# Kernel optimization log

Hardware: AMD Instinct MI355X
Metric: run time of the kernel (lower is better)

Reference implementation:

```python
import jax, jax.numpy as jnp
import numpy as np

TAU = 0.4
EPS = 1e-8


def setup_inputs() -> dict:
    key = jax.random.key(0)
    k1, k2 = jax.random.split(key)
    B, N, C, M = 4, 4096, 256, 2048
    l_feat = jax.random.normal(k1, (B, N, C), dtype=jnp.float32)
    g_feat = jax.random.normal(k2, (B, C, M), dtype=jnp.float32)
    return {"l_feat": l_feat, "g_feat": g_feat}


def reference(l_feat, g_feat):
    # l_feat: [B, N, C], g_feat: [B, C, M]
    # cosine similarity over channel dim C (torch CosineSimilarity, dim=2)
    l_norm = jnp.linalg.norm(l_feat, axis=2)          # [B, N]
    g_norm = jnp.linalg.norm(g_feat, axis=1)          # [B, M]
    dot = jnp.einsum('bnc,bcm->bnm', l_feat, g_feat)  # [B, N, M]
    cos_sim = dot / jnp.maximum(l_norm[:, :, None] * g_norm[:, None, :], EPS)
    sim = jnp.exp(cos_sim / TAU)                      # [B, N, M]
    # diag_embed(rowsum) followed by linalg.inv and bmm is exactly
    # row-wise division by the degree (row sum)
    sim = sim / jnp.sum(sim, axis=2, keepdims=True)
    # bmm(sim, g_feat^T): [B,N,M] x [B,M,C] -> [B,N,C]
    g_enh = jnp.einsum('bnm,bcm->bnc', sim, g_feat)
    return l_feat + g_enh
```

## Files before the change

kernel.cpp:

```cpp
#include <hip/hip_runtime.h>

#define B_ 4
#define N_ 4096
#define C_ 256
#define M_ 2048

typedef __attribute__((ext_vector_type(8))) short short8;
typedef __attribute__((ext_vector_type(4))) short short4v;
typedef __attribute__((ext_vector_type(4))) float f32x4;

union U16x8 { uint4 u4; unsigned short us[8]; short8 s8; };
union U16x4 { uint2 u2; unsigned short us[4]; short4v s4; };

__device__ __forceinline__ float bf2f(unsigned short h) {
    unsigned int u = ((unsigned int)h) << 16;
    return __builtin_bit_cast(float, u);
}
__device__ __forceinline__ unsigned short f2bf(float f) {
    unsigned int u = __builtin_bit_cast(unsigned int, f);
    u += 0x7FFFu + ((u >> 16) & 1u);
    return (unsigned short)(u >> 16);
}

#define GLB_AS(p) ((const __attribute__((address_space(1))) unsigned int*)(p))
#define LDS_AS(p) ((__attribute__((address_space(3))) unsigned int*)(p))

__device__ __forceinline__ f32x4 mfma16x16(short4v a, short4v b, f32x4 c) {
#if __has_builtin(__builtin_amdgcn_mfma_f32_16x16x16bf16_1k)
    return __builtin_amdgcn_mfma_f32_16x16x16bf16_1k(a, b, c, 0, 0, 0);
#else
    asm("v_mfma_f32_16x16x16_bf16 %0, %1, %2, %0" : "+v"(c) : "v"(a), "v"(b));
    return c;
#endif
}

__global__ __launch_bounds__(1024) void k_prep(const float* __restrict__ g,
                                               unsigned short* __restrict__ gcm,
                                               unsigned short* __restrict__ gmc) {
    __shared__ float red[16][64];
    __shared__ float sInv[64];
    __shared__ unsigned short T[64 * 66];
    const int b = blockIdx.y, m0 = blockIdx.x * 64;
    const int tid = threadIdx.x;
    const int ml = tid & 63, cq = tid >> 6;

    const float* gb = g + (size_t)b * C_ * M_ + m0 + ml;
    float ss = 0.f;
#pragma unroll 4
    for (int i = 0; i < 16; ++i) {
        float v = gb[(size_t)(cq * 16 + i) * M_];
        ss += v * v;
    }
    red[cq][ml] = ss;
    __syncthreads();
    if (cq == 0) {
        float t = 0.f;
#pragma unroll
        for (int k = 0; k < 16; ++k) t += red[k][ml];
        sInv[ml] = 1.f / fmaxf(sqrtf(t), 1e-8f);
    }
    __syncthreads();

    for (int c0 = 0; c0 < C_; c0 += 64) {
        const float* gbase = g + ((size_t)b * C_ + c0) * M_ + m0;
        unsigned short* gcmb = gcm + ((size_t)b * C_ + c0) * M_ + m0;
        {
            int id = tid;
            int ci = id >> 4, mq = (id & 15) * 4;
            float4 v = *(const float4*)(gbase + (size_t)ci * M_ + mq);
            uint2 pk;
            pk.x = (unsigned)f2bf(v.x) | ((unsigned)f2bf(v.y) << 16);
            pk.y = (unsigned)f2bf(v.z) | ((unsigned)f2bf(v.w) << 16);
            *(uint2*)(gcmb + (size_t)ci * M_ + mq) = pk;
            T[ci * 66 + mq + 0] = f2bf(v.x * sInv[mq + 0]);
            T[ci * 66 + mq + 1] = f2bf(v.y * sInv[mq + 1]);
            T[ci * 66 + mq + 2] = f2bf(v.z * sInv[mq + 2]);
            T[ci * 66 + mq + 3] = f2bf(v.w * sInv[mq + 3]);
        }
        __syncthreads();
        unsigned short* gmcb = gmc + ((size_t)b * M_ + m0) * C_ + c0;
        if (tid < 512) {
            int mr = tid >> 3, cc8 = (tid & 7) * 8;
            U16x8 t;
#pragma unroll
            for (int k = 0; k < 8; ++k) t.us[k] = T[(cc8 + k) * 66 + mr];
            *(uint4*)(gmcb + (size_t)mr * C_ + cc8) = t.u4;
        }
        __syncthreads();
    }
}

__global__ __launch_bounds__(512, 2) void k_main(
    const float* __restrict__ l,
    const unsigned short* __restrict__ gcm,
    const unsigned short* __restrict__ gmc,
    float* __restrict__ out)
{
    __shared__ __align__(16) char sMem[66560];
    unsigned short* sGmc = (unsigned short*)sMem;
    unsigned short* sGcm = (unsigned short*)(sMem + 32768);
    float (*sDen)[64] = (float (*)[64])(sMem + 65536);

    const int tid = threadIdx.x;
    const int w = tid >> 6;
    const int lane = tid & 63;
    const int l15 = lane & 15;
    const int quad = lane >> 4;
    const int kh = w & 3;
    const int rh = w >> 2;

    const int bid = blockIdx.x;
    const int xcd = bid & 7;
    const int b = xcd >> 1;
    const int row0 = (((bid >> 3) << 1) | (xcd & 1)) * 64;

    int goffA[4], goffB[4];
#pragma unroll
    for (int i = 0; i < 4; ++i) {
        int p = (w * 4 + i) * 64 + lane;
        int rA = p >> 5;
        goffA[i] = rA * 256 + (((p & 31) ^ (rA & 31)) << 3);
        int rB = p >> 3;
        goffB[i] = rB * 2048 + (((p & 7) ^ ((rB >> 1) & 7)) << 3);
    }

    const unsigned short* gmc_b = gmc + (size_t)b * M_ * C_;
    const unsigned short* gcm_b = gcm + (size_t)b * C_ * M_;

    auto dmaA = [&](int m0) {
#pragma unroll
        for (int i = 0; i < 4; ++i)
            __builtin_amdgcn_global_load_lds(GLB_AS(gmc_b + (size_t)m0 * 256 + goffA[i]),
                                             LDS_AS(&sGmc[(w * 4 + i) * 512]), 16, 0, 0);
    };
    auto dmaB = [&](int m0) {
#pragma unroll
        for (int i = 0; i < 4; ++i)
            __builtin_amdgcn_global_load_lds(GLB_AS(gcm_b + (size_t)m0 + goffB[i]),
                                             LDS_AS(&sGcm[(w * 4 + i) * 512]), 16, 0, 0);
    };

    dmaA(0);
    dmaB(0);

    short8 qf[2][8];
#pragma unroll
    for (int rt = 0; rt < 2; ++rt) {
        const float* lrow = l + ((size_t)b * N_ + row0 + rh * 32 + rt * 16 + l15) * C_;
        U16x8 qt[8];
        float ss = 0.f;
#pragma unroll
        for (int kk = 0; kk < 8; ++kk) {
            float4 x0 = *(const float4*)(lrow + kk * 32 + quad * 8);
            float4 x1 = *(const float4*)(lrow + kk * 32 + quad * 8 + 4);
            ss += x0.x*x0.x + x0.y*x0.y + x0.z*x0.z + x0.w*x0.w;
            ss += x1.x*x1.x + x1.y*x1.y + x1.z*x1.z + x1.w*x1.w;
            qt[kk].us[0] = f2bf(x0.x); qt[kk].us[1] = f2bf(x0.y);
            qt[kk].us[2] = f2bf(x0.z); qt[kk].us[3] = f2bf(x0.w);
            qt[kk].us[4] = f2bf(x1.x); qt[kk].us[5] = f2bf(x1.y);
            qt[kk].us[6] = f2bf(x1.z); qt[kk].us[7] = f2bf(x1.w);
        }
        ss += __shfl_xor(ss, 16);
        ss += __shfl_xor(ss, 32);
        const float invl = 1.0f / fmaxf(sqrtf(ss), 1e-8f);
#pragma unroll
        for (int kk = 0; kk < 8; ++kk) {
            U16x8 t;
#pragma unroll
            for (int j = 0; j < 8; ++j) t.us[j] = f2bf(bf2f(qt[kk].us[j]) * invl);
            qf[rt][kk] = t.s8;
        }
    }

    __syncthreads();

    f32x4 zero = {0.f, 0.f, 0.f, 0.f};
    f32x4 o[2][16];
#pragma unroll
    for (int i = 0; i < 2; ++i)
#pragma unroll
        for (int j = 0; j < 16; ++j) o[i][j] = zero;
    float dl0 = 0.f, dl1 = 0.f;

    const unsigned short* gAbase = &sGmc[(kh * 16 + l15) * 256];
    const int rxor = (kh * 16 + l15) & 31;
    const int chunkXor = (kh * 4 + quad) ^ (l15 & 14);
    const unsigned short* gBbase = &sGcm[l15 * 64 + (chunkXor << 2)];

    for (int mt = 0; mt < 32; ++mt) {
        f32x4 sa0 = zero, sa1 = zero;
#pragma unroll
        for (int kk = 0; kk < 8; ++kk) {
            short8 ag = *(const short8*)&gAbase[((kk * 4 + quad) ^ rxor) << 3];
            sa0 = __builtin_amdgcn_mfma_f32_16x16x32_bf16(ag, qf[0][kk], sa0, 0, 0, 0);
            sa1 = __builtin_amdgcn_mfma_f32_16x16x32_bf16(ag, qf[1][kk], sa1, 0, 0, 0);
        }
        U16x4 pk0, pk1;
#pragma unroll
        for (int r = 0; r < 4; ++r) {
            float p0 = exp2f(sa0[r] * 3.6067376022224085f);
            float p1 = exp2f(sa1[r] * 3.6067376022224085f);
            dl0 += p0; dl1 += p1;
            pk0.us[r] = f2bf(p0);
            pk1.us[r] = f2bf(p1);
        }
        __syncthreads();
        if (mt < 31) dmaA((mt + 1) * 64);

#pragma unroll
        for (int ct = 0; ct < 16; ++ct) {
            short4v bb = *(const short4v*)&gBbase[ct * 1024];
            o[0][ct] = mfma16x16(pk0.s4, bb, o[0][ct]);
            o[1][ct] = mfma16x16(pk1.s4, bb, o[1][ct]);
        }
        __syncthreads();
        if (mt < 31) dmaB((mt + 1) * 64);
    }

    {
        float d0 = dl0;
        d0 += __shfl_xor(d0, 16);
        d0 += __shfl_xor(d0, 32);
        float d1 = dl1;
        d1 += __shfl_xor(d1, 16);
        d1 += __shfl_xor(d1, 32);
        if (quad == 0) {
            sDen[kh][rh * 32 + l15] = d0;
            sDen[kh][rh * 32 + 16 + l15] = d1;
        }
    }

    f32x4* red4 = (f32x4*)sMem;
    const int wslot = kh * 1024 + quad * 16 + l15;
    const int rslot = (4 * kh) * 64 + quad * 16 + l15;
    f32x4 oacc0[4], oacc1[4];

#define RED_ROUND(RH, OSRC, ODST)                                              \
    __syncthreads();                                                           \
    if (rh == (RH)) {                                                          \
        _Pragma("unroll")                                                      \
        for (int j = 0; j < 16; ++j) red4[wslot + j * 64] = OSRC[j];           \
    }                                                                          \
    __syncthreads();                                                           \
    if (rh == (RH)) {                                                          \
        _Pragma("unroll")                                                      \
        for (int jj = 0; jj < 4; ++jj) {                                       \
            const int base = rslot + jj * 64;                                  \
            ODST[jj] = red4[base] + red4[base + 1024] +                        \
                       red4[base + 2048] + red4[base + 3072];                  \
        }                                                                      \
    }

    RED_ROUND(0, o[0], oacc0)
    RED_ROUND(0, o[1], oacc1)
    RED_ROUND(1, o[0], oacc0)
    RED_ROUND(1, o[1], oacc1)
#undef RED_ROUND

    const float* lb = l + ((size_t)b * N_ + row0 + rh * 32) * C_;
    float* ob = out + ((size_t)b * N_ + row0 + rh * 32) * C_;
#pragma unroll
    for (int r = 0; r < 4; ++r) {
        {
            const int row = quad * 4 + r;
            const int grow = rh * 32 + row;
            const float inv = 1.f / (sDen[0][grow] + sDen[1][grow] + sDen[2][grow] + sDen[3][grow]);
            const size_t rb = (size_t)row * C_;
#pragma unroll
            for (int jj = 0; jj < 4; ++jj) {
                const int c = kh * 64 + jj * 16 + l15;
                ob[rb + c] = lb[rb + c] + oacc0[jj][r] * inv;
            }
        }
        {
            const int row = 16 + quad * 4 + r;
            const int grow = rh * 32 + row;
            const float inv = 1.f / (sDen[0][grow] + sDen[1][grow] + sDen[2][grow] + sDen[3][grow]);
            const size_t rb = (size_t)row * C_;
#pragma unroll
            for (int jj = 0; jj < 4; ++jj) {
                const int c = kh * 64 + jj * 16 + l15;
                ob[rb + c] = lb[rb + c] + oacc1[jj][r] * inv;
            }
        }
    }
}

extern "C" void kernel_launch(void* const* d_in, const int* in_sizes, int n_in,
                              void* d_out, int out_size, void* d_ws, size_t ws_size,
                              hipStream_t stream) {
    (void)in_sizes; (void)n_in; (void)out_size; (void)ws_size;
    const float* l = (const float*)d_in[0];
    const float* g = (const float*)d_in[1];
    float* outp = (float*)d_out;

    char* ws = (char*)d_ws;
    unsigned short* gmc = (unsigned short*)ws;
    unsigned short* gcm = (unsigned short*)(ws + (size_t)B_ * M_ * C_ * 2);

    k_prep<<<dim3(M_ / 64, B_), 1024, 0, stream>>>(g, gcm, gmc);
    k_main<<<dim3(N_ / 64 * B_), 512, 0, stream>>>(l, gcm, gmc, outp);
}
```

Measured before the change: 136.9 us.

## Double-buffer LDS tiles and drop one barrier per iteration

Doubles the shared-memory staging so the next two m-tiles of g (both layouts) are prefetched into alternate buffers while the current tile is consumed. This removes the mid-iteration barrier and gives the async global-to-LDS loads a full iteration of lead time. The LDS footprint roughly doubles, so launch bounds drop to one block per CU. That gives up occupancy but allows more registers per thread, which matters little since the grid is only about one block per CU.

```diff
diff --git a/kernel.cpp b/kernel.cpp
--- a/kernel.cpp
+++ b/kernel.cpp
@@ -90,16 +90,16 @@
     }
 }
 
-__global__ __launch_bounds__(512, 2) void k_main(
+__global__ __launch_bounds__(512, 1) void k_main(
     const float* __restrict__ l,
     const unsigned short* __restrict__ gcm,
     const unsigned short* __restrict__ gmc,
     float* __restrict__ out)
 {
-    __shared__ __align__(16) char sMem[66560];
-    unsigned short* sGmc = (unsigned short*)sMem;
-    unsigned short* sGcm = (unsigned short*)(sMem + 32768);
-    float (*sDen)[64] = (float (*)[64])(sMem + 65536);
+    __shared__ __align__(16) char sMem[132096];
+    unsigned short* sGmcD = (unsigned short*)sMem;
+    unsigned short* sGcmD = (unsigned short*)(sMem + 65536);
+    float (*sDen)[64] = (float (*)[64])(sMem + 131072);
 
     const int tid = threadIdx.x;
     const int w = tid >> 6;
@@ -127,21 +127,23 @@
     const unsigned short* gmc_b = gmc + (size_t)b * M_ * C_;
     const unsigned short* gcm_b = gcm + (size_t)b * C_ * M_;
 
-    auto dmaA = [&](int m0) {
+    auto dmaA = [&](int tile, int buf) {
 #pragma unroll
         for (int i = 0; i < 4; ++i)
-            __builtin_amdgcn_global_load_lds(GLB_AS(gmc_b + (size_t)m0 * 256 + goffA[i]),
-                                             LDS_AS(&sGmc[(w * 4 + i) * 512]), 16, 0, 0);
+            __builtin_amdgcn_global_load_lds(GLB_AS(gmc_b + (size_t)tile * 16384 + goffA[i]),
+                                             LDS_AS(&sGmcD[buf * 16384 + (w * 4 + i) * 512]), 16, 0, 0);
     };
-    auto dmaB = [&](int m0) {
+    auto dmaB = [&](int tile, int buf) {
 #pragma unroll
         for (int i = 0; i < 4; ++i)
-            __builtin_amdgcn_global_load_lds(GLB_AS(gcm_b + (size_t)m0 + goffB[i]),
-                                             LDS_AS(&sGcm[(w * 4 + i) * 512]), 16, 0, 0);
+            __builtin_amdgcn_global_load_lds(GLB_AS(gcm_b + (size_t)tile * 64 + goffB[i]),
+                                             LDS_AS(&sGcmD[buf * 16384 + (w * 4 + i) * 512]), 16, 0, 0);
     };
 
-    dmaA(0);
-    dmaB(0);
+    dmaA(0, 0);
+    dmaB(0, 0);
+    dmaA(1, 1);
+    dmaB(1, 1);
 
     short8 qf[2][8];
 #pragma unroll
@@ -182,16 +184,20 @@
         for (int j = 0; j < 16; ++j) o[i][j] = zero;
     float dl0 = 0.f, dl1 = 0.f;
 
-    const unsigned short* gAbase = &sGmc[(kh * 16 + l15) * 256];
+    const unsigned short* gAbase = &sGmcD[(kh * 16 + l15) * 256];
     const int rxor = (kh * 16 + l15) & 31;
     const int chunkXor = (kh * 4 + quad) ^ (l15 & 14);
-    const unsigned short* gBbase = &sGcm[l15 * 64 + (chunkXor << 2)];
+    const unsigned short* gBbase = &sGcmD[l15 * 64 + (chunkXor << 2)];
 
     for (int mt = 0; mt < 32; ++mt) {
+        const int cur = mt & 1;
+        const unsigned short* gA = gAbase + cur * 16384;
+        const unsigned short* gB = gBbase + cur * 16384;
+
         f32x4 sa0 = zero, sa1 = zero;
 #pragma unroll
         for (int kk = 0; kk < 8; ++kk) {
-            short8 ag = *(const short8*)&gAbase[((kk * 4 + quad) ^ rxor) << 3];
+            short8 ag = *(const short8*)&gA[((kk * 4 + quad) ^ rxor) << 3];
             sa0 = __builtin_amdgcn_mfma_f32_16x16x32_bf16(ag, qf[0][kk], sa0, 0, 0, 0);
             sa1 = __builtin_amdgcn_mfma_f32_16x16x32_bf16(ag, qf[1][kk], sa1, 0, 0, 0);
         }
@@ -204,17 +210,19 @@
             pk0.us[r] = f2bf(p0);
             pk1.us[r] = f2bf(p1);
         }
-        __syncthreads();
-        if (mt < 31) dmaA((mt + 1) * 64);
 
 #pragma unroll
         for (int ct = 0; ct < 16; ++ct) {
-            short4v bb = *(const short4v*)&gBbase[ct * 1024];
+            short4v bb = *(const short4v*)&gB[ct * 1024];
             o[0][ct] = mfma16x16(pk0.s4, bb, o[0][ct]);
             o[1][ct] = mfma16x16(pk1.s4, bb, o[1][ct]);
         }
+
         __syncthreads();
-        if (mt < 31) dmaB((mt + 1) * 64);
+        if (mt < 30) {
+            dmaA(mt + 2, cur);
+            dmaB(mt + 2, cur);
+        }
     }
 
     {
```

New measurement: 144.0 us. +5.2%, slower.

## Use 1024-thread blocks with 16 rows per wave to halve register tiles

Applied to the files above, without the earlier changes.

Doubles k_main's block size to 16 waves so that each wave handles 16 query rows instead of 32. This halves per-wave accumulators, Q fragments and DMA work, and splits the cross-wave reduction into four rounds. The aim is lower register pressure and more waves to hide latency, at the cost of less reuse of each LDS B/A fragment per MFMA and more reduction barriers. The launch bounds of (1024,4) may force register spills, and LDS usage of 66.5KB per block caps residency.

```diff
diff --git a/kernel.cpp b/kernel.cpp
--- a/kernel.cpp
+++ b/kernel.cpp
@@ -90,7 +90,7 @@
     }
 }
 
-__global__ __launch_bounds__(512, 2) void k_main(
+__global__ __launch_bounds__(1024, 4) void k_main(
     const float* __restrict__ l,
     const unsigned short* __restrict__ gcm,
     const unsigned short* __restrict__ gmc,
@@ -114,10 +114,10 @@
     const int b = xcd >> 1;
     const int row0 = (((bid >> 3) << 1) | (xcd & 1)) * 64;
 
-    int goffA[4], goffB[4];
-#pragma unroll
-    for (int i = 0; i < 4; ++i) {
-        int p = (w * 4 + i) * 64 + lane;
+    int goffA[2], goffB[2];
+#pragma unroll
+    for (int i = 0; i < 2; ++i) {
+        int p = (w * 2 + i) * 64 + lane;
         int rA = p >> 5;
         goffA[i] = rA * 256 + (((p & 31) ^ (rA & 31)) << 3);
         int rB = p >> 3;
@@ -129,24 +129,23 @@
 
     auto dmaA = [&](int m0) {
 #pragma unroll
-        for (int i = 0; i < 4; ++i)
+        for (int i = 0; i < 2; ++i)
             __builtin_amdgcn_global_load_lds(GLB_AS(gmc_b + (size_t)m0 * 256 + goffA[i]),
-                                             LDS_AS(&sGmc[(w * 4 + i) * 512]), 16, 0, 0);
+                                             LDS_AS(&sGmc[(w * 2 + i) * 512]), 16, 0, 0);
     };
     auto dmaB = [&](int m0) {
 #pragma unroll
-        for (int i = 0; i < 4; ++i)
+        for (int i = 0; i < 2; ++i)
             __builtin_amdgcn_global_load_lds(GLB_AS(gcm_b + (size_t)m0 + goffB[i]),
-                                             LDS_AS(&sGcm[(w * 4 + i) * 512]), 16, 0, 0);
+                                             LDS_AS(&sGcm[(w * 2 + i) * 512]), 16, 0, 0);
     };
 
     dmaA(0);
     dmaB(0);
 
-    short8 qf[2][8];
-#pragma unroll
-    for (int rt = 0; rt < 2; ++rt) {
-        const float* lrow = l + ((size_t)b * N_ + row0 + rh * 32 + rt * 16 + l15) * C_;
+    short8 qf[8];
+    {
+        const float* lrow = l + ((size_t)b * N_ + row0 + rh * 16 + l15) * C_;
         U16x8 qt[8];
         float ss = 0.f;
 #pragma unroll
@@ -168,19 +167,17 @@
             U16x8 t;
 #pragma unroll
             for (int j = 0; j < 8; ++j) t.us[j] = f2bf(bf2f(qt[kk].us[j]) * invl);
-            qf[rt][kk] = t.s8;
+            qf[kk] = t.s8;
         }
     }
 
     __syncthreads();
 
     f32x4 zero = {0.f, 0.f, 0.f, 0.f};
-    f32x4 o[2][16];
-#pragma unroll
-    for (int i = 0; i < 2; ++i)
-#pragma unroll
-        for (int j = 0; j < 16; ++j) o[i][j] = zero;
-    float dl0 = 0.f, dl1 = 0.f;
+    f32x4 o[16];
+#pragma unroll
+    for (int j = 0; j < 16; ++j) o[j] = zero;
+    float dl = 0.f;
 
     const unsigned short* gAbase = &sGmc[(kh * 16 + l15) * 256];
     const int rxor = (kh * 16 + l15) & 31;
@@ -188,21 +185,18 @@
     const unsigned short* gBbase = &sGcm[l15 * 64 + (chunkXor << 2)];
 
     for (int mt = 0; mt < 32; ++mt) {
-        f32x4 sa0 = zero, sa1 = zero;
+        f32x4 sa = zero;
 #pragma unroll
         for (int kk = 0; kk < 8; ++kk) {
             short8 ag = *(const short8*)&gAbase[((kk * 4 + quad) ^ rxor) << 3];
-            sa0 = __builtin_amdgcn_mfma_f32_16x16x32_bf16(ag, qf[0][kk], sa0, 0, 0, 0);
-            sa1 = __builtin_amdgcn_mfma_f32_16x16x32_bf16(ag, qf[1][kk], sa1, 0, 0, 0);
-        }
-        U16x4 pk0, pk1;
+            sa = __builtin_amdgcn_mfma_f32_16x16x32_bf16(ag, qf[kk], sa, 0, 0, 0);
+        }
+        U16x4 pk;
 #pragma unroll
         for (int r = 0; r < 4; ++r) {
-            float p0 = exp2f(sa0[r] * 3.6067376022224085f);
-            float p1 = exp2f(sa1[r] * 3.6067376022224085f);
-            dl0 += p0; dl1 += p1;
-            pk0.us[r] = f2bf(p0);
-            pk1.us[r] = f2bf(p1);
+            float p = exp2f(sa[r] * 3.6067376022224085f);
+            dl += p;
+            pk.us[r] = f2bf(p);
         }
         __syncthreads();
         if (mt < 31) dmaA((mt + 1) * 64);
@@ -210,78 +204,58 @@
 #pragma unroll
         for (int ct = 0; ct < 16; ++ct) {
             short4v bb = *(const short4v*)&gBbase[ct * 1024];
-            o[0][ct] = mfma16x16(pk0.s4, bb, o[0][ct]);
-            o[1][ct] = mfma16x16(pk1.s4, bb, o[1][ct]);
+            o[ct] = mfma16x16(pk.s4, bb, o[ct]);
         }
         __syncthreads();
         if (mt < 31) dmaB((mt + 1) * 64);
     }
 
     {
-        float d0 = dl0;
-        d0 += __shfl_xor(d0, 16);
-        d0 += __shfl_xor(d0, 32);
-        float d1 = dl1;
-        d1 += __shfl_xor(d1, 16);
-        d1 += __shfl_xor(d1, 32);
-        if (quad == 0) {
-            sDen[kh][rh * 32 + l15] = d0;
-            sDen[kh][rh * 32 + 16 + l15] = d1;
-        }
+        float d = dl;
+        d += __shfl_xor(d, 16);
+        d += __shfl_xor(d, 32);
+        if (quad == 0) sDen[kh][rh * 16 + l15] = d;
     }
 
     f32x4* red4 = (f32x4*)sMem;
     const int wslot = kh * 1024 + quad * 16 + l15;
     const int rslot = (4 * kh) * 64 + quad * 16 + l15;
-    f32x4 oacc0[4], oacc1[4];
-
-#define RED_ROUND(RH, OSRC, ODST)                                              \
+    f32x4 oacc[4];
+
+#define RED_ROUND(RH)                                                          \
     __syncthreads();                                                           \
     if (rh == (RH)) {                                                          \
         _Pragma("unroll")                                                      \
-        for (int j = 0; j < 16; ++j) red4[wslot + j * 64] = OSRC[j];           \
+        for (int j = 0; j < 16; ++j) red4[wslot + j * 64] = o[j];              \
     }                                                                          \
     __syncthreads();                                                           \
     if (rh == (RH)) {                                                          \
         _Pragma("unroll")                                                      \
         for (int jj = 0; jj < 4; ++jj) {                                       \
             const int base = rslot + jj * 64;                                  \
-            ODST[jj] = red4[base] + red4[base + 1024] +                        \
+            oacc[jj] = red4[base] + red4[base + 1024] +                        \
                        red4[base + 2048] + red4[base + 3072];                  \
         }                                                                      \
     }
 
-    RED_ROUND(0, o[0], oacc0)
-    RED_ROUND(0, o[1], oacc1)
-    RED_ROUND(1, o[0], oacc0)
-    RED_ROUND(1, o[1], oacc1)
+    RED_ROUND(0)
+    RED_ROUND(1)
+    RED_ROUND(2)
+    RED_ROUND(3)
 #undef RED_ROUND
 
-    const float* lb = l + ((size_t)b * N_ + row0 + rh * 32) * C_;
-    float* ob = out + ((size_t)b * N_ + row0 + rh * 32) * C_;
+    const float* lb = l + ((size_t)b * N_ + row0 + rh * 16) * C_;
+    float* ob = out + ((size_t)b * N_ + row0 + rh * 16) * C_;
 #pragma unroll
     for (int r = 0; r < 4; ++r) {
-        {
-            const int row = quad * 4 + r;
-            const int grow = rh * 32 + row;
-            const float inv = 1.f / (sDen[0][grow] + sDen[1][grow] + sDen[2][grow] + sDen[3][grow]);
-            const size_t rb = (size_t)row * C_;
-#pragma unroll
-            for (int jj = 0; jj < 4; ++jj) {
-                const int c = kh * 64 + jj * 16 + l15;
-                ob[rb + c] = lb[rb + c] + oacc0[jj][r] * inv;
-            }
-        }
-        {
-            const int row = 16 + quad * 4 + r;
-            const int grow = rh * 32 + row;
-            const float inv = 1.f / (sDen[0][grow] + sDen[1][grow] + sDen[2][grow] + sDen[3][grow]);
-            const size_t rb = (size_t)row * C_;
-#pragma unroll
-            for (int jj = 0; jj < 4; ++jj) {
-                const int c = kh * 64 + jj * 16 + l15;
-                ob[rb + c] = lb[rb + c] + oacc1[jj][r] * inv;
-            }
+        const int row = quad * 4 + r;
+        const int grow = rh * 16 + row;
+        const float inv = 1.f / (sDen[0][grow] + sDen[1][grow] + sDen[2][grow] + sDen[3][grow]);
+        const size_t rb = (size_t)row * C_;
+#pragma unroll
+        for (int jj = 0; jj < 4; ++jj) {
+            const int c = kh * 64 + jj * 16 + l15;
+            ob[rb + c] = lb[rb + c] + oacc[jj][r] * inv;
         }
     }
 }
@@ -299,5 +273,5 @@
     unsigned short* gcm = (unsigned short*)(ws + (size_t)B_ * M_ * C_ * 2);
 
     k_prep<<<dim3(M_ / 64, B_), 1024, 0, stream>>>(g, gcm, gmc);
-    k_main<<<dim3(N_ / 64 * B_), 512, 0, stream>>>(l, gcm, gmc, outp);
-}
+    k_main<<<dim3(N_ / 64 * B_), 1024, 0, stream>>>(l, gcm, gmc, outp);
+}
```

Result: slower. 147.3 us (+7.7%).

## Pre-swizzle g into MFMA fragment layout and read operands directly from global

Applied to the files above, without the earlier changes.

The prep kernel now writes both bf16 copies of g in a layout blocked to match the MFMA fragment order. The main kernel drops the LDS staging (global_load_lds DMA plus two barriers per tile) and loads A and B fragments straight from global memory, relying on L2/L1 caching. This removes per-iteration synchronisation but exposes global load latency in the inner loop without explicit prefetch. Launch bounds are relaxed to one block per CU.

```diff
diff --git a/kernel.cpp b/kernel.cpp
--- a/kernel.cpp
+++ b/kernel.cpp
@@ -21,9 +21,6 @@
     u += 0x7FFFu + ((u >> 16) & 1u);
     return (unsigned short)(u >> 16);
 }
-
-#define GLB_AS(p) ((const __attribute__((address_space(1))) unsigned int*)(p))
-#define LDS_AS(p) ((__attribute__((address_space(3))) unsigned int*)(p))
 
 __device__ __forceinline__ f32x4 mfma16x16(short4v a, short4v b, f32x4 c) {
 #if __has_builtin(__builtin_amdgcn_mfma_f32_16x16x16bf16_1k)
@@ -35,8 +32,8 @@
 }
 
 __global__ __launch_bounds__(1024) void k_prep(const float* __restrict__ g,
-                                               unsigned short* __restrict__ gcm,
-                                               unsigned short* __restrict__ gmc) {
+                                               unsigned short* __restrict__ gcm2,
+                                               unsigned short* __restrict__ gmc2) {
     __shared__ float red[16][64];
     __shared__ float sInv[64];
     __shared__ unsigned short T[64 * 66];
@@ -61,44 +58,45 @@
     }
     __syncthreads();
 
+    unsigned short* gmc2b = gmc2 + (size_t)b * 524288 + (size_t)blockIdx.x * 16384;
+    unsigned short* gcm2b = gcm2 + (size_t)b * 524288 + (size_t)blockIdx.x * 16384;
+
     for (int c0 = 0; c0 < C_; c0 += 64) {
         const float* gbase = g + ((size_t)b * C_ + c0) * M_ + m0;
-        unsigned short* gcmb = gcm + ((size_t)b * C_ + c0) * M_ + m0;
         {
-            int id = tid;
-            int ci = id >> 4, mq = (id & 15) * 4;
+            int ci = tid >> 4, mq = (tid & 15) * 4;
             float4 v = *(const float4*)(gbase + (size_t)ci * M_ + mq);
             uint2 pk;
             pk.x = (unsigned)f2bf(v.x) | ((unsigned)f2bf(v.y) << 16);
             pk.y = (unsigned)f2bf(v.z) | ((unsigned)f2bf(v.w) << 16);
-            *(uint2*)(gcmb + (size_t)ci * M_ + mq) = pk;
+            const int cg = c0 + ci;
+            *(uint2*)(gcm2b + (cg >> 4) * 1024 + (mq >> 4) * 256 + (cg & 15) * 16 +
+                      ((mq >> 2) & 3) * 4) = pk;
             T[ci * 66 + mq + 0] = f2bf(v.x * sInv[mq + 0]);
             T[ci * 66 + mq + 1] = f2bf(v.y * sInv[mq + 1]);
             T[ci * 66 + mq + 2] = f2bf(v.z * sInv[mq + 2]);
             T[ci * 66 + mq + 3] = f2bf(v.w * sInv[mq + 3]);
         }
         __syncthreads();
-        unsigned short* gmcb = gmc + ((size_t)b * M_ + m0) * C_ + c0;
         if (tid < 512) {
             int mr = tid >> 3, cc8 = (tid & 7) * 8;
-            U16x8 t;
-#pragma unroll
-            for (int k = 0; k < 8; ++k) t.us[k] = T[(cc8 + k) * 66 + mr];
-            *(uint4*)(gmcb + (size_t)mr * C_ + cc8) = t.u4;
+            U16x8 t8;
+#pragma unroll
+            for (int k = 0; k < 8; ++k) t8.us[k] = T[(cc8 + k) * 66 + mr];
+            const int cg = c0 + cc8;
+            *(uint4*)(gmc2b + (cg >> 5) * 2048 + mr * 32 + ((cg >> 3) & 3) * 8) = t8.u4;
         }
         __syncthreads();
     }
 }
 
-__global__ __launch_bounds__(512, 2) void k_main(
+__global__ __launch_bounds__(512, 1) void k_main(
     const float* __restrict__ l,
-    const unsigned short* __restrict__ gcm,
-    const unsigned short* __restrict__ gmc,
+    const unsigned short* __restrict__ gcm2,
+    const unsigned short* __restrict__ gmc2,
     float* __restrict__ out)
 {
     __shared__ __align__(16) char sMem[66560];
-    unsigned short* sGmc = (unsigned short*)sMem;
-    unsigned short* sGcm = (unsigned short*)(sMem + 32768);
     float (*sDen)[64] = (float (*)[64])(sMem + 65536);
 
     const int tid = threadIdx.x;
@@ -114,34 +112,8 @@
     const int b = xcd >> 1;
     const int row0 = (((bid >> 3) << 1) | (xcd & 1)) * 64;
 
-    int goffA[4], goffB[4];
-#pragma unroll
-    for (int i = 0; i < 4; ++i) {
-        int p = (w * 4 + i) * 64 + lane;
-        int rA = p >> 5;
-        goffA[i] = rA * 256 + (((p & 31) ^ (rA & 31)) << 3);
-        int rB = p >> 3;
-        goffB[i] = rB * 2048 + (((p & 7) ^ ((rB >> 1) & 7)) << 3);
-    }
-
-    const unsigned short* gmc_b = gmc + (size_t)b * M_ * C_;
-    const unsigned short* gcm_b = gcm + (size_t)b * C_ * M_;
-
-    auto dmaA = [&](int m0) {
-#pragma unroll
-        for (int i = 0; i < 4; ++i)
-            __builtin_amdgcn_global_load_lds(GLB_AS(gmc_b + (size_t)m0 * 256 + goffA[i]),
-                                             LDS_AS(&sGmc[(w * 4 + i) * 512]), 16, 0, 0);
-    };
-    auto dmaB = [&](int m0) {
-#pragma unroll
-        for (int i = 0; i < 4; ++i)
-            __builtin_amdgcn_global_load_lds(GLB_AS(gcm_b + (size_t)m0 + goffB[i]),
-                                             LDS_AS(&sGcm[(w * 4 + i) * 512]), 16, 0, 0);
-    };
-
-    dmaA(0);
-    dmaB(0);
+    const unsigned short* gmc2_b = gmc2 + (size_t)b * 524288;
+    const unsigned short* gcm2_b = gcm2 + (size_t)b * 524288;
 
     short8 qf[2][8];
 #pragma unroll
@@ -172,8 +144,6 @@
         }
     }
 
-    __syncthreads();
-
     f32x4 zero = {0.f, 0.f, 0.f, 0.f};
     f32x4 o[2][16];
 #pragma unroll
@@ -182,16 +152,17 @@
         for (int j = 0; j < 16; ++j) o[i][j] = zero;
     float dl0 = 0.f, dl1 = 0.f;
 
-    const unsigned short* gAbase = &sGmc[(kh * 16 + l15) * 256];
-    const int rxor = (kh * 16 + l15) & 31;
-    const int chunkXor = (kh * 4 + quad) ^ (l15 & 14);
-    const unsigned short* gBbase = &sGcm[l15 * 64 + (chunkXor << 2)];
+    const unsigned short* gAbase = gmc2_b + (kh * 16 + l15) * 32 + quad * 8;
+    const unsigned short* gBbase = gcm2_b + kh * 256 + l15 * 16 + quad * 4;
 
     for (int mt = 0; mt < 32; ++mt) {
+        const unsigned short* gA = gAbase + (size_t)mt * 16384;
+        const unsigned short* gB = gBbase + (size_t)mt * 16384;
+
         f32x4 sa0 = zero, sa1 = zero;
 #pragma unroll
         for (int kk = 0; kk < 8; ++kk) {
-            short8 ag = *(const short8*)&gAbase[((kk * 4 + quad) ^ rxor) << 3];
+            short8 ag = *(const short8*)&gA[kk * 2048];
             sa0 = __builtin_amdgcn_mfma_f32_16x16x32_bf16(ag, qf[0][kk], sa0, 0, 0, 0);
             sa1 = __builtin_amdgcn_mfma_f32_16x16x32_bf16(ag, qf[1][kk], sa1, 0, 0, 0);
         }
@@ -204,17 +175,13 @@
             pk0.us[r] = f2bf(p0);
             pk1.us[r] = f2bf(p1);
         }
-        __syncthreads();
-        if (mt < 31) dmaA((mt + 1) * 64);
 
 #pragma unroll
         for (int ct = 0; ct < 16; ++ct) {
-            short4v bb = *(const short4v*)&gBbase[ct * 1024];
+            short4v bb = *(const short4v*)&gB[ct * 1024];
             o[0][ct] = mfma16x16(pk0.s4, bb, o[0][ct]);
             o[1][ct] = mfma16x16(pk1.s4, bb, o[1][ct]);
         }
-        __syncthreads();
-        if (mt < 31) dmaB((mt + 1) * 64);
     }
 
     {
@@ -295,9 +262,9 @@
     float* outp = (float*)d_out;
 
     char* ws = (char*)d_ws;
-    unsigned short* gmc = (unsigned short*)ws;
-    unsigned short* gcm = (unsigned short*)(ws + (size_t)B_ * M_ * C_ * 2);
-
-    k_prep<<<dim3(M_ / 64, B_), 1024, 0, stream>>>(g, gcm, gmc);
-    k_main<<<dim3(N_ / 64 * B_), 512, 0, stream>>>(l, gcm, gmc, outp);
-}
+    unsigned short* gmc2 = (unsigned short*)ws;
+    unsigned short* gcm2 = (unsigned short*)(ws + (size_t)B_ * M_ * C_ * 2);
+
+    k_prep<<<dim3(M_ / 64, B_), 1024, 0, stream>>>(g, gcm2, gmc2);
+    k_main<<<dim3(N_ / 64 * B_), 512, 0, stream>>>(l, gcm2, gmc2, outp);
+}
```

Measured after the change: 159.5 us. 1.17x slower.
